# Kernel optimization log

Measured on AMD Instinct MI355X. Metric: run time of the kernel, lower is better.

## Reference

```python
import jax, jax.numpy as jnp
import numpy as np

B, L, U, H = 16, 1024, 512, 2  # batch, seq_len, units, highway_num


def setup_inputs() -> dict:
    key = jax.random.key(0)
    ks = jax.random.split(key, 8)
    s = 0.02  # weight init scale
    return {
        "inputs": jax.random.normal(ks[0], (B, L, U), dtype=jnp.float32),
        "tW": jax.random.normal(ks[1], (H, U, U), dtype=jnp.float32) * s,
        "tb": jnp.zeros((H, U), dtype=jnp.float32),
        "cW": jax.random.normal(ks[2], (H, U, U), dtype=jnp.float32) * s,
        "cb": jnp.zeros((H, U), dtype=jnp.float32),
        "aW": jax.random.normal(ks[3], (3 * U,), dtype=jnp.float32) * s,
        "ab": jnp.zeros((1,), dtype=jnp.float32),
        "frW": jax.random.normal(ks[4], (2 * U, U), dtype=jnp.float32) * s,
        "frb": jnp.zeros((U,), dtype=jnp.float32),
        "ffW": jax.random.normal(ks[5], (2 * U, U), dtype=jnp.float32) * s,
        "ffb": jnp.zeros((U,), dtype=jnp.float32),
    }


def reference(inputs, tW, tb, cW, cb, aW, ab, frW, frb, ffW, ffb):
    # Highway stack (inference: dropout is identity)
    x = inputs
    for i in range(tW.shape[0]):
        t = jax.nn.relu(x @ tW[i] + tb[i])
        c = jax.nn.sigmoid(x @ cW[i] + cb[i])
        x = t * c + x * (1.0 - c)

    # Pairwise MLP self-attention.
    # Original: A_ij = relu(dense1(concat([x_i, x_j, x_i*x_j]))).
    # Split aW = [w1; w2; w3] so we never materialize the [B,L,L,3U] tensor:
    # A_ij = relu(x_i.w1 + x_j.w2 + sum_d x_i_d * x_j_d * w3_d + b)
    u = x.shape[-1]
    w1, w2, w3 = aW[:u], aW[u:2 * u], aW[2 * u:]
    s1 = x @ w1                                    # [B,L]
    s2 = x @ w2                                    # [B,L]
    s3 = jnp.einsum('bid,bjd->bij', x * w3, x)     # [B,L,L]
    A = jax.nn.relu(s1[:, :, None] + s2[:, None, :] + s3 + ab[0])
    att = jnp.einsum('bij,bjd->bid', jax.nn.softmax(A, axis=-1), x)

    # Fuse gate. NOTE: original code uses fuse_f_dense (sigmoid) for BOTH
    # z and f (fuse_z_dense is never called), so z == f at inference.
    concat = jnp.concatenate([inputs, att], axis=-1)  # [B,L,2U]
    z = jax.nn.sigmoid(concat @ ffW + ffb)
    r = jax.nn.sigmoid(concat @ frW + frb)
    f = z
    return r * inputs + f * z
```

## Files before the change

kernel.cpp:

```cpp
#include <hip/hip_runtime.h>
#include <math.h>

typedef __bf16 bf16;
typedef __attribute__((ext_vector_type(8))) __bf16 bf16x8;
typedef __attribute__((ext_vector_type(4))) float f32x4;

#define CDIV(a,b) (((a)+(b)-1)/(b))


__device__ __forceinline__ void load_lds16(const bf16* g, bf16* l) {
  __builtin_amdgcn_global_load_lds(
      (const __attribute__((address_space(1))) unsigned int*)(g),
      (__attribute__((address_space(3))) unsigned int*)(l), 16, 0, 0);
}

struct GemmArgs {
  const bf16* A; const bf16* B; bf16* C;
  int K, lda, ldb, ldc;
  long long Ab, Bb, Cb;
  const float* bias;
  const float* s1; const float* s2; const float* abp;
  int L;
  int gxsh, gysh;
};

template<int EPI>
__global__ __launch_bounds__(256, 4)
void gemm_nt(GemmArgs g) {
  __shared__ bf16 As[128 * 64];
  __shared__ bf16 Bs[128 * 64];
  const int tid = threadIdx.x;

  const int bid = blockIdx.x;
  const int xcd = bid & 7;
  const int t = bid >> 3;
  const int bx = t & ((1 << g.gxsh) - 1);
  const int r  = t >> g.gxsh;
  const int Rx = gridDim.x >> (3 + g.gxsh);
  const int gr = xcd * Rx + r;
  const int by = gr & ((1 << g.gysh) - 1);
  const int bz = gr >> g.gysh;

  const bf16* Ag = g.A + (long long)bz * g.Ab + (long long)(by * 128) * g.lda;
  const bf16* Bg = g.B + (long long)bz * g.Bb + (long long)(bx * 128) * g.ldb;
  const int wid = tid >> 6, lane = tid & 63;
  const int wm = (wid >> 1) << 6;
  const int wn = (wid & 1) << 6;
  const int lr = lane & 15, lq = lane >> 4;

  f32x4 acc[4][4];
#pragma unroll
  for (int i = 0; i < 4; i++)
#pragma unroll
    for (int j = 0; j < 4; j++) acc[i][j] = f32x4{0.f, 0.f, 0.f, 0.f};

  const int srow8 = (tid >> 3) & 7;
  const int skc   = (tid & 7) ^ srow8;
  const int lswz  = (lr & 7);

  for (int k0 = 0; k0 < g.K; k0 += 64) {
    __syncthreads();
#pragma unroll
    for (int j = 0; j < 4; j++) {
      const int ci = (tid >> 6) * 4 + j;
      const int row = ci * 8 + srow8;
      load_lds16(Ag + (long long)row * g.lda + k0 + skc * 8, As + ci * 512);
      load_lds16(Bg + (long long)row * g.ldb + k0 + skc * 8, Bs + ci * 512);
    }
    __syncthreads();
#pragma unroll
    for (int ks = 0; ks < 2; ks++) {
      bf16x8 af[4], bfr[4];
      const int kx = (ks * 4 + lq) ^ lswz;
#pragma unroll
      for (int i = 0; i < 4; i++)
        af[i] = *(const bf16x8*)(&As[(wm + i * 16 + lr) * 64 + kx * 8]);
#pragma unroll
      for (int j = 0; j < 4; j++)
        bfr[j] = *(const bf16x8*)(&Bs[(wn + j * 16 + lr) * 64 + kx * 8]);
#pragma unroll
      for (int i = 0; i < 4; i++)
#pragma unroll
        for (int j = 0; j < 4; j++)
          acc[i][j] = __builtin_amdgcn_mfma_f32_16x16x32_bf16(af[i], bfr[j], acc[i][j], 0, 0, 0);
    }
  }

  bf16* Cg = g.C + (long long)bz * g.Cb;
#pragma unroll
  for (int i = 0; i < 4; i++) {
#pragma unroll
    for (int v = 0; v < 4; v++) {
      int row = by * 128 + wm + i * 16 + lq * 4 + v;
      float srow = 0.f;
      if (EPI == 1) srow = g.s1[bz * g.L + row] + g.abp[0];
#pragma unroll
      for (int j = 0; j < 4; j++) {
        int col = bx * 128 + wn + j * 16 + lr;
        float val = acc[i][j][v];
        if (EPI == 0) val += g.bias[col];
        if (EPI == 1) { val += srow + g.s2[bz * g.L + col]; val = fmaxf(val, 0.f); }
        if (EPI == 3) { val += g.bias[col]; val = 1.f / (1.f + __expf(-val)); }
        Cg[(long long)row * g.ldc + col] = (bf16)val;
      }
    }
  }
}

__global__ void wprep(const float* tW, const float* tb, const float* cW, const float* cb,
                      const float* frW, const float* frb, const float* ffW, const float* ffb,
                      bf16* w1T, bf16* w2T, float* bias1, float* bias2) {
  int idx = blockIdx.x * 256 + threadIdx.x;
  const int N1 = 1048576, N2 = 1048576;
  if (idx < N1) {
    int l = idx >> 19;
    int rem = idx & 524287;
    int n = rem >> 9, k = rem & 511;
    float v = (n < 512) ? tW[l * 262144 + k * 512 + n]
                        : cW[l * 262144 + k * 512 + (n - 512)];
    w1T[idx] = (bf16)v;
  } else if (idx < N1 + N2) {
    int j = idx - N1;
    int n = j >> 10, k = j & 1023;
    float v = (n < 512) ? ffW[k * 512 + n] : frW[k * 512 + (n - 512)];
    w2T[j] = (bf16)v;
  } else if (idx < N1 + N2 + 3072) {
    int j = idx - (N1 + N2);
    if (j < 2048) {
      int l = j >> 10, n = j & 1023;
      bias1[j] = (n < 512) ? tb[l * 512 + n] : cb[l * 512 + (n - 512)];
    } else {
      int n = j - 2048;
      bias2[n] = (n < 512) ? ffb[n] : frb[n - 512];
    }
  }
}

__global__ void init_conv(const float* inp, bf16* xb, bf16* cat16) {
  long long i8 = ((long long)blockIdx.x * 256 + threadIdx.x) * 8;
  int m = (int)(i8 >> 9), u = (int)(i8 & 511);
  bf16x8 o;
#pragma unroll
  for (int k = 0; k < 8; k++) o[k] = (bf16)inp[i8 + k];
  *(bf16x8*)(xb + i8) = o;
  *(bf16x8*)(cat16 + (long long)m * 1024 + u) = o;
}

__global__ void highway_ew(const bf16* pre, const bf16* xin, bf16* xout) {
  long long i8 = ((long long)blockIdx.x * 256 + threadIdx.x) * 8;
  int m = (int)(i8 >> 9), u = (int)(i8 & 511);
  bf16x8 t8 = *(const bf16x8*)(pre + (long long)m * 1024 + u);
  bf16x8 c8 = *(const bf16x8*)(pre + (long long)m * 1024 + 512 + u);
  bf16x8 x8 = *(const bf16x8*)(xin + i8);
  bf16x8 o;
#pragma unroll
  for (int k = 0; k < 8; k++) {
    float t = fmaxf((float)t8[k], 0.f);
    float c = 1.f / (1.f + __expf(-(float)c8[k]));
    float x = (float)x8[k];
    o[k] = (bf16)(t * c + x * (1.f - c));
  }
  *(bf16x8*)(xout + i8) = o;
}

__global__ void s1s2_k(const bf16* xb, const float* aW, float* s1, float* s2) {
  int wid = threadIdx.x >> 6, lane = threadIdx.x & 63;
  int m = blockIdx.x * 4 + wid;
  const bf16* row = xb + (long long)m * 512;
  float a1 = 0.f, a2 = 0.f;
#pragma unroll
  for (int i = 0; i < 8; i++) {
    int d = lane + i * 64;
    float x = (float)row[d];
    a1 += x * aW[d];
    a2 += x * aW[512 + d];
  }
  for (int off = 32; off; off >>= 1) {
    a1 += __shfl_down(a1, off, 64);
    a2 += __shfl_down(a2, off, 64);
  }
  if (!lane) { s1[m] = a1; s2[m] = a2; }
}

__global__ void q16_k(const bf16* xb, const float* w3, bf16* q16) {
  long long i8 = ((long long)blockIdx.x * 256 + threadIdx.x) * 8;
  int d = (int)(i8 & 511);
  bf16x8 xv = *(const bf16x8*)(xb + i8);
  bf16x8 o;
#pragma unroll
  for (int k = 0; k < 8; k++) o[k] = (bf16)((float)xv[k] * w3[d + k]);
  *(bf16x8*)(q16 + i8) = o;
}

__global__ __launch_bounds__(256) void transpose_k(const bf16* xb, bf16* xT) {
  __shared__ bf16 t[64][65];
  int b = blockIdx.z;
  int d0 = blockIdx.x * 64, j0 = blockIdx.y * 64;
  const bf16* src = xb + (long long)b * 524288;
  bf16* dst = xT + (long long)b * 524288;
  int tid = threadIdx.x;
  int rr = tid >> 3, cc = (tid & 7) * 8;
#pragma unroll
  for (int it = 0; it < 2; ++it) {
    int r = rr + it * 32;
    bf16x8 v = *(const bf16x8*)(src + (long long)(j0 + r) * 512 + d0 + cc);
#pragma unroll
    for (int k = 0; k < 8; k++) t[cc + k][r] = v[k];
  }
  __syncthreads();
#pragma unroll
  for (int it = 0; it < 2; ++it) {
    int r = rr + it * 32;
    bf16x8 v;
#pragma unroll
    for (int k = 0; k < 8; k++) v[k] = t[r][cc + k];
    *(bf16x8*)(dst + (long long)(d0 + r) * 1024 + j0 + cc) = v;
  }
}

__global__ __launch_bounds__(256) void softmax_k(bf16* S) {
  __shared__ float red[8];
  long long base = (long long)blockIdx.x * 1024;
  int tid = threadIdx.x, lane = tid & 63, wid = tid >> 6;
  float v[4];
#pragma unroll
  for (int i = 0; i < 4; i++) v[i] = (float)S[base + tid + 256 * i];
  float m = fmaxf(fmaxf(v[0], v[1]), fmaxf(v[2], v[3]));
  for (int off = 32; off; off >>= 1) m = fmaxf(m, __shfl_down(m, off, 64));
  if (!lane) red[wid] = m;
  __syncthreads();
  m = fmaxf(fmaxf(red[0], red[1]), fmaxf(red[2], red[3]));
  float e[4], s = 0.f;
#pragma unroll
  for (int i = 0; i < 4; i++) { e[i] = __expf(v[i] - m); s += e[i]; }
  for (int off = 32; off; off >>= 1) s += __shfl_down(s, off, 64);
  if (!lane) red[4 + wid] = s;
  __syncthreads();
  float inv = 1.f / (red[4] + red[5] + red[6] + red[7]);
#pragma unroll
  for (int i = 0; i < 4; i++) S[base + tid + 256 * i] = (bf16)(e[i] * inv);
}

__global__ void final_out(const bf16* pre, const float* inp, float* out) {
  long long i8 = ((long long)blockIdx.x * 256 + threadIdx.x) * 8;
  int m = (int)(i8 >> 9), u = (int)(i8 & 511);
  bf16x8 z8 = *(const bf16x8*)(pre + (long long)m * 1024 + u);
  bf16x8 r8 = *(const bf16x8*)(pre + (long long)m * 1024 + 512 + u);
  f32x4 o0, o1;
#pragma unroll
  for (int k = 0; k < 8; k++) {
    float z = (float)z8[k], r = (float)r8[k];
    float x = inp[i8 + k];
    float val = r * x + z * z;
    if (k < 4) o0[k] = val; else o1[k - 4] = val;
  }
  *(f32x4*)(out + i8) = o0;
  *(f32x4*)(out + i8 + 4) = o1;
}

extern "C" void kernel_launch(void* const* d_in, const int* in_sizes, int n_in,
                              void* d_out, int out_size, void* d_ws, size_t ws_size,
                              hipStream_t stream) {
  const float* inp = (const float*)d_in[0];
  const float* tW  = (const float*)d_in[1];
  const float* tb  = (const float*)d_in[2];
  const float* cW  = (const float*)d_in[3];
  const float* cb  = (const float*)d_in[4];
  const float* aW  = (const float*)d_in[5];
  const float* ab  = (const float*)d_in[6];
  const float* frW = (const float*)d_in[7];
  const float* frb = (const float*)d_in[8];
  const float* ffW = (const float*)d_in[9];
  const float* ffb = (const float*)d_in[10];
  float* out = (float*)d_out;

  char* p = (char*)d_ws;
  auto alloc = [&](size_t bytes) { char* r = p; p += (bytes + 255) & ~size_t(255); return r; };
  bf16* xb    = (bf16*) alloc(16777216);
  bf16* q16   = (bf16*) alloc(16777216);
  bf16* xT16  = (bf16*) alloc(16777216);
  bf16* cat16 = (bf16*) alloc(33554432);
  bf16* preS  = (bf16*) alloc(33554432);
  float* s1   = (float*)alloc(65536);
  float* s2   = (float*)alloc(65536);
  bf16* w1T   = (bf16*) alloc(2097152);
  bf16* w2T   = (bf16*) alloc(2097152);
  float* bias1= (float*)alloc(8192);
  float* bias2= (float*)alloc(4096);

  wprep<<<CDIV(1048576 + 1048576 + 3072, 256), 256, 0, stream>>>(
      tW, tb, cW, cb, frW, frb, ffW, ffb, w1T, w2T, bias1, bias2);
  init_conv<<<4096, 256, 0, stream>>>(inp, xb, cat16);

  for (int l = 0; l < 2; l++) {
    GemmArgs g{};
    g.A = xb; g.B = w1T + (long long)l * 524288; g.C = preS;
    g.K = 512; g.lda = 512; g.ldb = 512; g.ldc = 1024;
    g.Ab = g.Bb = g.Cb = 0; g.bias = bias1 + l * 1024;
    g.gxsh = 3; g.gysh = 7;
    gemm_nt<0><<<1024, 256, 0, stream>>>(g);
    highway_ew<<<4096, 256, 0, stream>>>(preS, xb, xb);
  }

  s1s2_k<<<4096, 256, 0, stream>>>(xb, aW, s1, s2);
  q16_k<<<4096, 256, 0, stream>>>(xb, aW + 1024, q16);
  transpose_k<<<dim3(8, 16, 16), 256, 0, stream>>>(xb, xT16);

  {
    GemmArgs g{};
    g.A = q16; g.B = xb; g.C = preS;
    g.K = 512; g.lda = 512; g.ldb = 512; g.ldc = 1024;
    g.Ab = 524288; g.Bb = 524288; g.Cb = 1048576;
    g.s1 = s1; g.s2 = s2; g.abp = ab; g.L = 1024;
    g.gxsh = 3; g.gysh = 3;
    gemm_nt<1><<<1024, 256, 0, stream>>>(g);
  }
  softmax_k<<<16384, 256, 0, stream>>>(preS);
  {
    GemmArgs g{};
    g.A = preS; g.B = xT16; g.C = cat16 + 512;
    g.K = 1024; g.lda = 1024; g.ldb = 1024; g.ldc = 1024;
    g.Ab = 1048576; g.Bb = 524288; g.Cb = 1048576;
    g.gxsh = 2; g.gysh = 3;
    gemm_nt<2><<<512, 256, 0, stream>>>(g);
  }
  {
    GemmArgs g{};
    g.A = cat16; g.B = w2T; g.C = preS;
    g.K = 1024; g.lda = 1024; g.ldb = 1024; g.ldc = 1024;
    g.Ab = g.Bb = g.Cb = 0; g.bias = bias2;
    g.gxsh = 3; g.gysh = 7;
    gemm_nt<3><<<1024, 256, 0, stream>>>(g);
  }
  final_out<<<4096, 256, 0, stream>>>(preS, inp, out);
}
```

Before: 315.9 us.

## Fuse highway and output gate elementwise epilogues into paired-column dual GEMMs

Adds a gemm_dual kernel whose B tile interleaves matching columns from the two weight halves (t/c or z/r), so one block holds both pre-activations and applies the highway update or the final gate directly in the epilogue. This removes the highway_ew and final_out kernels and their round trip through the bf16 preS buffer. The final GEMM reads inputs and attention from two separate buffers instead of a concatenated one, and s1/s2 and q16 are computed in one pass. Each dual-GEMM block now covers 64 output columns rather than 128, which changes reuse, and the final output is computed from fp32 accumulators without an intermediate bf16 rounding.

```diff
diff --git a/kernel.cpp b/kernel.cpp
--- a/kernel.cpp
+++ b/kernel.cpp
@@ -18,7 +18,6 @@
   const bf16* A; const bf16* B; bf16* C;
   int K, lda, ldb, ldc;
   long long Ab, Bb, Cb;
-  const float* bias;
   const float* s1; const float* s2; const float* abp;
   int L;
   int gxsh, gysh;
@@ -30,7 +29,6 @@
   __shared__ bf16 As[128 * 64];
   __shared__ bf16 Bs[128 * 64];
   const int tid = threadIdx.x;
-
   const int bid = blockIdx.x;
   const int xcd = bid & 7;
   const int t = bid >> 3;
@@ -98,10 +96,106 @@
       for (int j = 0; j < 4; j++) {
         int col = bx * 128 + wn + j * 16 + lr;
         float val = acc[i][j][v];
-        if (EPI == 0) val += g.bias[col];
         if (EPI == 1) { val += srow + g.s2[bz * g.L + col]; val = fmaxf(val, 0.f); }
-        if (EPI == 3) { val += g.bias[col]; val = 1.f / (1.f + __expf(-val)); }
         Cg[(long long)row * g.ldc + col] = (bf16)val;
+      }
+    }
+  }
+}
+
+struct DualArgs {
+  const bf16* A; const bf16* A2;
+  const bf16* Bt;
+  void* C; const void* xres;
+  const float* bias_t; const float* bias_c;
+  int K, ldb;
+};
+
+template<int EPI>
+__global__ __launch_bounds__(256, 4)
+void gemm_dual(DualArgs g) {
+  __shared__ bf16 As[128 * 64];
+  __shared__ bf16 Bs[128 * 64];
+  const int tid = threadIdx.x;
+  const int bid = blockIdx.x;
+  const int xcd = bid & 7;
+  const int t = bid >> 3;
+  const int bx = t & 7;
+  const int r  = t >> 3;
+  const int Rx = gridDim.x >> 6;
+  const int by = xcd * Rx + r;
+
+  const int wid = tid >> 6, lane = tid & 63;
+  const int wm = (wid >> 1) << 6;
+  const int wn = (wid & 1) << 6;
+  const int lr = lane & 15, lq = lane >> 4;
+
+  f32x4 acc[4][4];
+#pragma unroll
+  for (int i = 0; i < 4; i++)
+#pragma unroll
+    for (int j = 0; j < 4; j++) acc[i][j] = f32x4{0.f, 0.f, 0.f, 0.f};
+
+  const int srow8 = (tid >> 3) & 7;
+  const int skc   = (tid & 7) ^ srow8;
+  const int lswz  = (lr & 7);
+  const long long abase = (long long)(by * 128) * 512;
+
+  for (int k0 = 0; k0 < g.K; k0 += 64) {
+    const bf16* Ak = (k0 < 512) ? g.A : g.A2;
+    const int kk = k0 & 511;
+    __syncthreads();
+#pragma unroll
+    for (int j = 0; j < 4; j++) {
+      const int ci = (tid >> 6) * 4 + j;
+      const int bn = ci * 8 + srow8;
+      load_lds16(Ak + abase + (long long)bn * 512 + kk + skc * 8, As + ci * 512);
+      const int grp = bn >> 5, r5 = bn & 31;
+      const int grow = ((grp & 1) << 9) + bx * 64 + ((grp >> 1) << 5) + r5;
+      load_lds16(g.Bt + (long long)grow * g.ldb + k0 + skc * 8, Bs + ci * 512);
+    }
+    __syncthreads();
+#pragma unroll
+    for (int ks = 0; ks < 2; ks++) {
+      bf16x8 af[4], bfr[4];
+      const int kx = (ks * 4 + lq) ^ lswz;
+#pragma unroll
+      for (int i = 0; i < 4; i++)
+        af[i] = *(const bf16x8*)(&As[(wm + i * 16 + lr) * 64 + kx * 8]);
+#pragma unroll
+      for (int j = 0; j < 4; j++)
+        bfr[j] = *(const bf16x8*)(&Bs[(wn + j * 16 + lr) * 64 + kx * 8]);
+#pragma unroll
+      for (int i = 0; i < 4; i++)
+#pragma unroll
+        for (int j = 0; j < 4; j++)
+          acc[i][j] = __builtin_amdgcn_mfma_f32_16x16x32_bf16(af[i], bfr[j], acc[i][j], 0, 0, 0);
+    }
+  }
+
+  const int colb = bx * 64 + (wn >> 1);
+#pragma unroll
+  for (int i = 0; i < 4; i++) {
+#pragma unroll
+    for (int v = 0; v < 4; v++) {
+      int row = by * 128 + wm + i * 16 + lq * 4 + v;
+#pragma unroll
+      for (int j = 0; j < 2; j++) {
+        int col = colb + j * 16 + lr;
+        long long idx = (long long)row * 512 + col;
+        float p0 = acc[i][j][v] + g.bias_t[col];
+        float p1 = acc[i][j + 2][v] + g.bias_c[col];
+        if (EPI == 0) {
+          float tt = fmaxf(p0, 0.f);
+          float c = 1.f / (1.f + __expf(-p1));
+          float x = (float)((const bf16*)g.xres)[idx];
+          ((bf16*)g.C)[idx] = (bf16)(tt * c + x * (1.f - c));
+        } else {
+          float z = 1.f / (1.f + __expf(-p0));
+          float rr = 1.f / (1.f + __expf(-p1));
+          float x = ((const float*)g.xres)[idx];
+          ((float*)g.C)[idx] = rr * x + z * z;
+        }
       }
     }
   }
@@ -136,60 +230,35 @@
   }
 }
 
-__global__ void init_conv(const float* inp, bf16* xb, bf16* cat16) {
+__global__ void init_conv(const float* inp, bf16* xb0) {
   long long i8 = ((long long)blockIdx.x * 256 + threadIdx.x) * 8;
-  int m = (int)(i8 >> 9), u = (int)(i8 & 511);
   bf16x8 o;
 #pragma unroll
   for (int k = 0; k < 8; k++) o[k] = (bf16)inp[i8 + k];
-  *(bf16x8*)(xb + i8) = o;
-  *(bf16x8*)(cat16 + (long long)m * 1024 + u) = o;
-}
-
-__global__ void highway_ew(const bf16* pre, const bf16* xin, bf16* xout) {
-  long long i8 = ((long long)blockIdx.x * 256 + threadIdx.x) * 8;
-  int m = (int)(i8 >> 9), u = (int)(i8 & 511);
-  bf16x8 t8 = *(const bf16x8*)(pre + (long long)m * 1024 + u);
-  bf16x8 c8 = *(const bf16x8*)(pre + (long long)m * 1024 + 512 + u);
-  bf16x8 x8 = *(const bf16x8*)(xin + i8);
-  bf16x8 o;
-#pragma unroll
-  for (int k = 0; k < 8; k++) {
-    float t = fmaxf((float)t8[k], 0.f);
-    float c = 1.f / (1.f + __expf(-(float)c8[k]));
-    float x = (float)x8[k];
-    o[k] = (bf16)(t * c + x * (1.f - c));
-  }
-  *(bf16x8*)(xout + i8) = o;
-}
-
-__global__ void s1s2_k(const bf16* xb, const float* aW, float* s1, float* s2) {
+  *(bf16x8*)(xb0 + i8) = o;
+}
+
+__global__ void s1s2q_k(const bf16* x, const float* aW, float* s1, float* s2, bf16* q16) {
   int wid = threadIdx.x >> 6, lane = threadIdx.x & 63;
   int m = blockIdx.x * 4 + wid;
-  const bf16* row = xb + (long long)m * 512;
+  long long base = (long long)m * 512;
+  int d0 = lane * 8;
+  bf16x8 xv = *(const bf16x8*)(x + base + d0);
   float a1 = 0.f, a2 = 0.f;
-#pragma unroll
-  for (int i = 0; i < 8; i++) {
-    int d = lane + i * 64;
-    float x = (float)row[d];
-    a1 += x * aW[d];
-    a2 += x * aW[512 + d];
-  }
+  bf16x8 o;
+#pragma unroll
+  for (int k = 0; k < 8; k++) {
+    float xx = (float)xv[k];
+    a1 += xx * aW[d0 + k];
+    a2 += xx * aW[512 + d0 + k];
+    o[k] = (bf16)(xx * aW[1024 + d0 + k]);
+  }
+  *(bf16x8*)(q16 + base + d0) = o;
   for (int off = 32; off; off >>= 1) {
     a1 += __shfl_down(a1, off, 64);
     a2 += __shfl_down(a2, off, 64);
   }
   if (!lane) { s1[m] = a1; s2[m] = a2; }
-}
-
-__global__ void q16_k(const bf16* xb, const float* w3, bf16* q16) {
-  long long i8 = ((long long)blockIdx.x * 256 + threadIdx.x) * 8;
-  int d = (int)(i8 & 511);
-  bf16x8 xv = *(const bf16x8*)(xb + i8);
-  bf16x8 o;
-#pragma unroll
-  for (int k = 0; k < 8; k++) o[k] = (bf16)((float)xv[k] * w3[d + k]);
-  *(bf16x8*)(q16 + i8) = o;
 }
 
 __global__ __launch_bounds__(256) void transpose_k(const bf16* xb, bf16* xT) {
@@ -239,23 +308,6 @@
   float inv = 1.f / (red[4] + red[5] + red[6] + red[7]);
 #pragma unroll
   for (int i = 0; i < 4; i++) S[base + tid + 256 * i] = (bf16)(e[i] * inv);
-}
-
-__global__ void final_out(const bf16* pre, const float* inp, float* out) {
-  long long i8 = ((long long)blockIdx.x * 256 + threadIdx.x) * 8;
-  int m = (int)(i8 >> 9), u = (int)(i8 & 511);
-  bf16x8 z8 = *(const bf16x8*)(pre + (long long)m * 1024 + u);
-  bf16x8 r8 = *(const bf16x8*)(pre + (long long)m * 1024 + 512 + u);
-  f32x4 o0, o1;
-#pragma unroll
-  for (int k = 0; k < 8; k++) {
-    float z = (float)z8[k], r = (float)r8[k];
-    float x = inp[i8 + k];
-    float val = r * x + z * z;
-    if (k < 4) o0[k] = val; else o1[k - 4] = val;
-  }
-  *(f32x4*)(out + i8) = o0;
-  *(f32x4*)(out + i8 + 4) = o1;
 }
 
 extern "C" void kernel_launch(void* const* d_in, const int* in_sizes, int n_in,
@@ -276,10 +328,12 @@
 
   char* p = (char*)d_ws;
   auto alloc = [&](size_t bytes) { char* r = p; p += (bytes + 255) & ~size_t(255); return r; };
-  bf16* xb    = (bf16*) alloc(16777216);
+  bf16* xb0   = (bf16*) alloc(16777216);
+  bf16* x1    = (bf16*) alloc(16777216);
+  bf16* x2    = (bf16*) alloc(16777216);
   bf16* q16   = (bf16*) alloc(16777216);
   bf16* xT16  = (bf16*) alloc(16777216);
-  bf16* cat16 = (bf16*) alloc(33554432);
+  bf16* att16 = (bf16*) alloc(16777216);
   bf16* preS  = (bf16*) alloc(33554432);
   float* s1   = (float*)alloc(65536);
   float* s2   = (float*)alloc(65536);
@@ -290,25 +344,27 @@
 
   wprep<<<CDIV(1048576 + 1048576 + 3072, 256), 256, 0, stream>>>(
       tW, tb, cW, cb, frW, frb, ffW, ffb, w1T, w2T, bias1, bias2);
-  init_conv<<<4096, 256, 0, stream>>>(inp, xb, cat16);
-
-  for (int l = 0; l < 2; l++) {
-    GemmArgs g{};
-    g.A = xb; g.B = w1T + (long long)l * 524288; g.C = preS;
-    g.K = 512; g.lda = 512; g.ldb = 512; g.ldc = 1024;
-    g.Ab = g.Bb = g.Cb = 0; g.bias = bias1 + l * 1024;
-    g.gxsh = 3; g.gysh = 7;
-    gemm_nt<0><<<1024, 256, 0, stream>>>(g);
-    highway_ew<<<4096, 256, 0, stream>>>(preS, xb, xb);
-  }
-
-  s1s2_k<<<4096, 256, 0, stream>>>(xb, aW, s1, s2);
-  q16_k<<<4096, 256, 0, stream>>>(xb, aW + 1024, q16);
-  transpose_k<<<dim3(8, 16, 16), 256, 0, stream>>>(xb, xT16);
+  init_conv<<<4096, 256, 0, stream>>>(inp, xb0);
+
+  {
+    const bf16* xin[2] = {xb0, x1};
+    bf16* xout[2] = {x1, x2};
+    for (int l = 0; l < 2; l++) {
+      DualArgs g{};
+      g.A = xin[l]; g.A2 = xin[l]; g.Bt = w1T + (long long)l * 524288;
+      g.C = xout[l]; g.xres = xin[l];
+      g.bias_t = bias1 + l * 1024; g.bias_c = bias1 + l * 1024 + 512;
+      g.K = 512; g.ldb = 512;
+      gemm_dual<0><<<1024, 256, 0, stream>>>(g);
+    }
+  }
+
+  s1s2q_k<<<4096, 256, 0, stream>>>(x2, aW, s1, s2, q16);
+  transpose_k<<<dim3(8, 16, 16), 256, 0, stream>>>(x2, xT16);
 
   {
     GemmArgs g{};
-    g.A = q16; g.B = xb; g.C = preS;
+    g.A = q16; g.B = x2; g.C = preS;
     g.K = 512; g.lda = 512; g.ldb = 512; g.ldc = 1024;
     g.Ab = 524288; g.Bb = 524288; g.Cb = 1048576;
     g.s1 = s1; g.s2 = s2; g.abp = ab; g.L = 1024;
@@ -318,19 +374,18 @@
   softmax_k<<<16384, 256, 0, stream>>>(preS);
   {
     GemmArgs g{};
-    g.A = preS; g.B = xT16; g.C = cat16 + 512;
-    g.K = 1024; g.lda = 1024; g.ldb = 1024; g.ldc = 1024;
-    g.Ab = 1048576; g.Bb = 524288; g.Cb = 1048576;
+    g.A = preS; g.B = xT16; g.C = att16;
+    g.K = 1024; g.lda = 1024; g.ldb = 1024; g.ldc = 512;
+    g.Ab = 1048576; g.Bb = 524288; g.Cb = 524288;
     g.gxsh = 2; g.gysh = 3;
     gemm_nt<2><<<512, 256, 0, stream>>>(g);
   }
   {
-    GemmArgs g{};
-    g.A = cat16; g.B = w2T; g.C = preS;
-    g.K = 1024; g.lda = 1024; g.ldb = 1024; g.ldc = 1024;
-    g.Ab = g.Bb = g.Cb = 0; g.bias = bias2;
-    g.gxsh = 3; g.gysh = 7;
-    gemm_nt<3><<<1024, 256, 0, stream>>>(g);
-  }
-  final_out<<<4096, 256, 0, stream>>>(preS, inp, out);
-}
+    DualArgs g{};
+    g.A = xb0; g.A2 = att16; g.Bt = w2T;
+    g.C = out; g.xres = inp;
+    g.bias_t = bias2; g.bias_c = bias2 + 512;
+    g.K = 1024; g.ldb = 1024;
+    gemm_dual<1><<<1024, 256, 0, stream>>>(g);
+  }
+}
```

Measured after the change: 291.1 us. 1.09x faster.
